# Performance work log

Hardware: AMD Instinct MI355X
Metric: run time of the kernel (lower is better)

## Reference

```python
import jax, jax.numpy as jnp
import numpy as np

N_NODES = 50000
N_EDGES = 800000
IN_CH = 256
HID = 64
OUT_CH = 64
N_LAYERS = 3
ALPHA = 0.1


def _gpr_temp():
    t = ALPHA * (1.0 - ALPHA) ** np.arange(N_LAYERS + 1)
    t[-1] = (1.0 - ALPHA) ** N_LAYERS
    return jnp.asarray(t, dtype=jnp.float32)


def setup_inputs() -> dict:
    key = jax.random.key(0)
    ks = jax.random.split(key, 8)
    x = jax.random.normal(ks[0], (N_NODES, IN_CH), dtype=jnp.float32)
    edge_index = jax.random.randint(ks[1], (2, N_EDGES), 0, N_NODES, dtype=jnp.int64 if jax.config.jax_enable_x64 else jnp.int32).astype(jnp.int32)
    edge_w = jax.random.uniform(ks[2], (N_EDGES,), dtype=jnp.float32)
    # xavier-uniform-ish scales
    W_in = jax.random.normal(ks[3], (IN_CH, HID), dtype=jnp.float32) * (1.0 / np.sqrt(IN_CH))
    b_in = jnp.zeros((HID,), dtype=jnp.float32)
    layer_W = jax.random.normal(ks[4], (N_LAYERS, HID, HID), dtype=jnp.float32) * (1.0 / np.sqrt(HID))
    layer_b = jnp.zeros((N_LAYERS, HID), dtype=jnp.float32)
    W_out = jax.random.normal(ks[5], (HID, OUT_CH), dtype=jnp.float32) * (1.0 / np.sqrt(HID))
    b_out = jnp.zeros((OUT_CH,), dtype=jnp.float32)
    temp = _gpr_temp()
    return {"x": x, "edge_index": edge_index, "edge_w": edge_w, "W_in": W_in,
            "b_in": b_in, "layer_W": layer_W, "layer_b": layer_b,
            "W_out": W_out, "b_out": b_out, "temp": temp}


def reference(x, edge_index, edge_w, W_in, b_in, layer_W, layer_b, W_out, b_out, temp):
    src, dst = edge_index[0], edge_index[1]
    # inlinear
    h = x @ W_in + b_in                      # [N, HID]
    # GPR combination: hidden = sum_k temp[k] * relu(SpMM(linear(h_k)))
    hidden = h * temp[0]
    cur = h
    for i in range(layer_W.shape[0]):
        z = cur @ layer_W[i] + layer_b[i]    # [N, HID]
        m = z[src] * edge_w[:, None]         # gather + edge weight, [E, HID]
        agg = jax.ops.segment_sum(m, dst, num_segments=x.shape[0])  # scatter-sum
        cur = jax.nn.relu(agg)               # dropout is identity in eval mode
        hidden = hidden + cur * temp[i + 1]
    return hidden @ W_out + b_out            # [N, OUT_CH]
```

## Files before the change

kernel.cpp:

```cpp
#include <hip/hip_runtime.h>
#include <hip/hip_bf16.h>

#define NN 50000
#define NE 800000
#define CIN 256
#define HH 64
#define NBINS 196
#define B1 256
#define EPB 3125
#define NGB 782
#define NLB 3125

typedef unsigned long long u64;
typedef __attribute__((ext_vector_type(8))) short short8;
typedef __attribute__((ext_vector_type(4))) float f32x4;

__device__ __forceinline__ float bf2f(ushort u) {
    union { unsigned int i; float f; } v; v.i = ((unsigned int)u) << 16; return v.f;
}
__device__ __forceinline__ ushort f2bf(float f) {
    __hip_bfloat16 b = __float2bfloat16(f);
    return *reinterpret_cast<ushort*>(&b);
}

__global__ __launch_bounds__(256) void k_prep(
    const float* __restrict__ W_in, const float* __restrict__ LW,
    const float* __restrict__ W_out, ushort* __restrict__ Wp)
{
    const int tid = blockIdx.x * 256 + threadIdx.x;
    if (tid < 16384) {
        const int i = tid & 7;
        const int l = (tid >> 3) & 63;
        const int s = (tid >> 9) & 7;
        const int t = tid >> 12;
        const int k = s * 32 + (l >> 4) * 8 + i;
        const int c = t * 16 + (l & 15);
        Wp[tid] = f2bf(W_in[k * HH + c]);
    } else {
        const int q = (tid - 16384) & 4095;
        const int m = (tid - 16384) >> 12;
        const int i = q & 7;
        const int l = (q >> 3) & 63;
        const int s = (q >> 9) & 1;
        const int t = q >> 10;
        const int k = s * 32 + (l >> 4) * 8 + i;
        const int c = t * 16 + (l & 15);
        const float* Wm = (m < 3) ? (LW + m * HH * HH) : W_out;
        Wp[tid] = f2bf(Wm[k * HH + c]);
    }
}

__global__ __launch_bounds__(256) void k_fused(
    const float* __restrict__ x, const ushort* __restrict__ Wp,
    const float* __restrict__ b, const int* __restrict__ dst,
    int* __restrict__ H, ushort* __restrict__ h_bf)
{
    __shared__ int hist[NBINS];
    if (blockIdx.x < B1) {
        for (int t = threadIdx.x; t < NBINS; t += 256) hist[t] = 0;
        __syncthreads();
        const int e0 = blockIdx.x * EPB;
        for (int i = threadIdx.x; i < EPB; i += 256)
            atomicAdd(&hist[dst[e0 + i] >> 8], 1);
        __syncthreads();
        for (int t = threadIdx.x; t < NBINS; t += 256)
            H[t * B1 + blockIdx.x] = hist[t];
        return;
    }
    const int w = threadIdx.x >> 6;
    const int l = threadIdx.x & 63;
    const int R0 = (blockIdx.x - B1) * 64 + w * 16;
    const int arow = R0 + (l & 15);
    const int xrow = (arow < NN) ? arow : (NN - 1);
    const float* xr = x + (size_t)xrow * CIN + (l >> 4) * 8;
    const short8* WpV = (const short8*)Wp;

    f32x4 acc0 = {0,0,0,0}, acc1 = {0,0,0,0}, acc2 = {0,0,0,0}, acc3 = {0,0,0,0};
    #pragma unroll
    for (int s = 0; s < 8; ++s) {
        const float4 xa = *(const float4*)(xr + s * 32);
        const float4 xb = *(const float4*)(xr + s * 32 + 4);
        short8 af;
        af[0] = (short)f2bf(xa.x); af[1] = (short)f2bf(xa.y);
        af[2] = (short)f2bf(xa.z); af[3] = (short)f2bf(xa.w);
        af[4] = (short)f2bf(xb.x); af[5] = (short)f2bf(xb.y);
        af[6] = (short)f2bf(xb.z); af[7] = (short)f2bf(xb.w);
        acc0 = __builtin_amdgcn_mfma_f32_16x16x32_bf16(af, WpV[(0*8+s)*64 + l], acc0, 0, 0, 0);
        acc1 = __builtin_amdgcn_mfma_f32_16x16x32_bf16(af, WpV[(1*8+s)*64 + l], acc1, 0, 0, 0);
        acc2 = __builtin_amdgcn_mfma_f32_16x16x32_bf16(af, WpV[(2*8+s)*64 + l], acc2, 0, 0, 0);
        acc3 = __builtin_amdgcn_mfma_f32_16x16x32_bf16(af, WpV[(3*8+s)*64 + l], acc3, 0, 0, 0);
    }
    const int colb = l & 15;
    const int rbase = R0 + (l >> 4) * 4;
    #pragma unroll
    for (int t = 0; t < 4; ++t) {
        const f32x4 a = (t == 0) ? acc0 : (t == 1) ? acc1 : (t == 2) ? acc2 : acc3;
        const float bb = b[t * 16 + colb];
        #pragma unroll
        for (int r = 0; r < 4; ++r) {
            const int row = rbase + r;
            if (row < NN)
                h_bf[(size_t)row * HH + t * 16 + colb] = f2bf(a[r] + bb);
        }
    }
}

__global__ __launch_bounds__(256) void k_scanH(
    int* __restrict__ H, int* __restrict__ Sx, int* __restrict__ bcnt)
{
    __shared__ int s[256];
    const int t = threadIdx.x;
    int rowsum = 0;
    if (t < NBINS) {
        const int4* row = (const int4*)(H + t * B1);
        #pragma unroll 8
        for (int c = 0; c < B1 / 4; ++c) {
            const int4 v = row[c];
            rowsum += v.x + v.y + v.z + v.w;
        }
    }
    s[t] = (t < NBINS) ? rowsum : 0;
    __syncthreads();
    #pragma unroll
    for (int off = 1; off < 256; off <<= 1) {
        const int add = (t >= off) ? s[t - off] : 0;
        __syncthreads();
        s[t] += add;
        __syncthreads();
    }
    if (t < NBINS) {
        const int rowstart = s[t] - rowsum;
        Sx[t] = rowstart;
        bcnt[t] = rowsum;
        int run = rowstart;
        int4* row = (int4*)(H + t * B1);
        for (int c = 0; c < B1 / 4; ++c) {
            int4 v = row[c];
            int4 o;
            o.x = run; run += v.x;
            o.y = run; run += v.y;
            o.z = run; run += v.z;
            o.w = run; run += v.w;
            row[c] = o;
        }
    }
}

__global__ __launch_bounds__(256) void k_scatterA(
    const int* __restrict__ src, const int* __restrict__ dst,
    const float* __restrict__ ew, const int* __restrict__ H,
    int2* __restrict__ tmp_e, ushort* __restrict__ tmp_low)
{
    __shared__ int cur[NBINS];
    for (int t = threadIdx.x; t < NBINS; t += 256)
        cur[t] = H[t * B1 + blockIdx.x];
    __syncthreads();
    const int e0 = blockIdx.x * EPB;
    for (int i = threadIdx.x; i < EPB; i += 256) {
        const int e = e0 + i;
        const int d = dst[e];
        const int pos = atomicAdd(&cur[d >> 8], 1);
        tmp_e[pos] = make_int2(src[e], __float_as_int(ew[e]));
        tmp_low[pos] = (ushort)(d & 255);
    }
}

__global__ __launch_bounds__(512) void k_sortB(
    const int2* __restrict__ tmp_e, const ushort* __restrict__ tmp_low,
    const int* __restrict__ Sx, const int* __restrict__ bcnt,
    int2* __restrict__ epack, int* __restrict__ rowptr, int* __restrict__ cnt)
{
    __shared__ int hist[256], s[256], curs[256];
    const int b = blockIdx.x;
    const int base = Sx[b];
    const int cntE = bcnt[b];
    const int t = threadIdx.x;
    if (t < 256) hist[t] = 0;
    __syncthreads();
    for (int i = t; i < cntE; i += 512)
        atomicAdd(&hist[tmp_low[base + i]], 1);
    __syncthreads();
    if (t < 256) s[t] = hist[t];
    __syncthreads();
    #pragma unroll
    for (int off = 1; off < 256; off <<= 1) {
        const int add = (t < 256 && t >= off) ? s[t - off] : 0;
        __syncthreads();
        if (t < 256) s[t] += add;
        __syncthreads();
    }
    if (t < 256) {
        const int excl = s[t] - hist[t];
        curs[t] = excl;
        const int d = b * 256 + t;
        if (d < NN) { rowptr[d] = base + excl; cnt[d] = hist[t]; }
    }
    __syncthreads();
    for (int i = t; i < cntE; i += 512) {
        const int2 e = tmp_e[base + i];
        const int low = (int)tmp_low[base + i];
        const int pos = base + atomicAdd(&curs[low], 1);
        epack[pos] = e;
    }
}

template<bool FINAL>
__global__ __launch_bounds__(256) void k_layer(
    const ushort* __restrict__ cur_in, ushort* __restrict__ cur_out,
    const int2* __restrict__ epack, const int* __restrict__ rowptr,
    const int* __restrict__ cnt,
    const ushort* __restrict__ WpL, const float* __restrict__ bvec,
    const float* __restrict__ temp,
    const ushort* __restrict__ hbf, const ushort* __restrict__ c1,
    const ushort* __restrict__ WpO, const float* __restrict__ bout,
    float* __restrict__ outp)
{
    __shared__ int2  es[4][64];
    __shared__ ushort ts[16][72];
    __shared__ float swv[16];
    const int w = threadIdx.x >> 6;
    const int j = threadIdx.x & 63;
    const int nb = blockIdx.x * 16;

    #pragma unroll
    for (int q = 0; q < 4; ++q) {
        const int n  = nb + w * 4 + q;
        const int rs = rowptr[n];
        const int rc = cnt[n];
        float acc = 0.0f;
        float sw  = 0.0f;
        for (int base = 0; base < rc; base += 64) {
            const int m = min(rc - base, 64);
            if (j < m) es[w][j] = epack[rs + base + j];
            for (int g = 0; g < m; g += 8) {
                float vv[8], ww[8];
                #pragma unroll
                for (int u = 0; u < 8; ++u) {
                    const int idx = g + u;
                    const int sel = (idx < m) ? idx : 0;
                    const int2 p = es[w][sel];
                    ww[u] = (idx < m) ? __int_as_float(p.y) : 0.0f;
                    vv[u] = bf2f(cur_in[(size_t)p.x * HH + j]);
                }
                #pragma unroll
                for (int u = 0; u < 8; ++u) { acc = fmaf(ww[u], vv[u], acc); sw += ww[u]; }
            }
        }
        ts[w * 4 + q][j] = f2bf(acc);
        if (j == 0) swv[w * 4 + q] = sw;
    }
    __syncthreads();

    const int lr = j & 15;
    const int lg = j >> 4;
    const short8 a0 = *(const short8*)&ts[lr][lg * 8];
    const short8 a1 = *(const short8*)&ts[lr][32 + lg * 8];
    if (FINAL) __syncthreads();

    const short8* WpV = (const short8*)WpL;
    f32x4 zac = {0,0,0,0};
    zac = __builtin_amdgcn_mfma_f32_16x16x32_bf16(a0, WpV[(w*2+0)*64 + j], zac, 0, 0, 0);
    zac = __builtin_amdgcn_mfma_f32_16x16x32_bf16(a1, WpV[(w*2+1)*64 + j], zac, 0, 0, 0);

    const float bb = bvec[w * 16 + lr];
    float t0v = 0, t1v = 0, t2v = 0, t3v = 0;
    if (FINAL) { t0v = temp[0]; t1v = temp[1]; t2v = temp[2]; t3v = temp[3]; }
    #pragma unroll
    for (int r = 0; r < 4; ++r) {
        const int row = lg * 4 + r;
        const int n   = nb + row;
        const float z = zac[r] + swv[row] * bb;
        const float rv = fmaxf(z, 0.0f);
        const size_t o = (size_t)n * HH + w * 16 + lr;
        if (!FINAL) {
            cur_out[o] = f2bf(rv);
        } else {
            const float hid = t0v * bf2f(hbf[o]) + t1v * bf2f(c1[o])
                            + t2v * bf2f(cur_in[o]) + t3v * rv;
            ts[row][w * 16 + lr] = f2bf(hid);
        }
    }
    if (FINAL) {
        __syncthreads();
        const short8 b0 = *(const short8*)&ts[lr][lg * 8];
        const short8 b1 = *(const short8*)&ts[lr][32 + lg * 8];
        const short8* WoV = (const short8*)WpO;
        f32x4 oz = {0,0,0,0};
        oz = __builtin_amdgcn_mfma_f32_16x16x32_bf16(b0, WoV[(w*2+0)*64 + j], oz, 0, 0, 0);
        oz = __builtin_amdgcn_mfma_f32_16x16x32_bf16(b1, WoV[(w*2+1)*64 + j], oz, 0, 0, 0);
        const float bo = bout[w * 16 + lr];
        #pragma unroll
        for (int r = 0; r < 4; ++r) {
            const int row = lg * 4 + r;
            outp[(size_t)(nb + row) * HH + w * 16 + lr] = oz[r] + bo;
        }
    }
}

extern "C" void kernel_launch(void* const* d_in, const int* in_sizes, int n_in,
                              void* d_out, int out_size, void* d_ws, size_t ws_size,
                              hipStream_t stream)
{
    const float* x     = (const float*)d_in[0];
    const int*   ei    = (const int*)d_in[1];
    const float* ew    = (const float*)d_in[2];
    const float* W_in  = (const float*)d_in[3];
    const float* b_in  = (const float*)d_in[4];
    const float* LW    = (const float*)d_in[5];
    const float* Lb    = (const float*)d_in[6];
    const float* W_out = (const float*)d_in[7];
    const float* b_out = (const float*)d_in[8];
    const float* temp  = (const float*)d_in[9];
    const int* src = ei;
    const int* dst = ei + NE;

    char* p = (char*)d_ws;
    ushort* h_bf    = (ushort*)p;  p += (size_t)NN * HH * 2;
    ushort* curA    = (ushort*)p;  p += (size_t)NN * HH * 2;
    ushort* curB    = (ushort*)p;  p += (size_t)NN * HH * 2;
    int2*   epack   = (int2*)p;    p += (size_t)NE * 8;
    int2*   tmp_e   = (int2*)p;    p += (size_t)NE * 8;
    ushort* tmp_low = (ushort*)p;  p += (size_t)NE * 2;
    int*    H       = (int*)p;     p += (size_t)NBINS * B1 * 4;
    int*    Sx      = (int*)p;     p += (NBINS + 1) * 4;
    int*    bcnt    = (int*)p;     p += NBINS * 4;
    int*    rowptr  = (int*)p;     p += (size_t)NN * 4;
    int*    cnt     = (int*)p;     p += (size_t)NN * 4;
    ushort* Wp      = (ushort*)p;  p += 32768 * 2;
    float*  out     = (float*)d_out;

    const ushort* WpIn  = Wp;
    const ushort* WpL0  = Wp + 16384;
    const ushort* WpL1  = Wp + 16384 + 4096;
    const ushort* WpL2  = Wp + 16384 + 2 * 4096;
    const ushort* WpOut = Wp + 16384 + 3 * 4096;

    k_prep<<<128, 256, 0, stream>>>(W_in, LW, W_out, Wp);
    k_fused<<<B1 + NGB, 256, 0, stream>>>(x, WpIn, b_in, dst, H, h_bf);
    k_scanH<<<1, 256, 0, stream>>>(H, Sx, bcnt);
    k_scatterA<<<B1, 256, 0, stream>>>(src, dst, ew, H, tmp_e, tmp_low);
    k_sortB<<<NBINS, 512, 0, stream>>>(tmp_e, tmp_low, Sx, bcnt, epack, rowptr, cnt);

    k_layer<false><<<NLB, 256, 0, stream>>>(h_bf, curA, epack, rowptr, cnt,
                                            WpL0, Lb + 0 * HH, temp,
                                            nullptr, nullptr, nullptr, nullptr, nullptr);
    k_layer<false><<<NLB, 256, 0, stream>>>(curA, curB, epack, rowptr, cnt,
                                            WpL1, Lb + 1 * HH, temp,
                                            nullptr, nullptr, nullptr, nullptr, nullptr);
    k_layer<true><<<NLB, 256, 0, stream>>>(curB, nullptr, epack, rowptr, cnt,
                                           WpL2, Lb + 2 * HH, temp,
                                           h_bf, curA, WpOut, b_out, out);
}
```

Before: 159.0 us.

## Parallelize histogram row scan across blocks and prefetch edge packs in layer kernel

The single-block scan that serially wrote per-bin offsets over 256 entries per thread is split in two. A one-block pass now computes only bin totals and starts, and a second 196-block pass does a parallel block-wide prefix scan of each histogram row. In the layer kernel, row pointers and counts for all four nodes are loaded up front, and each node's first 64 edge records are prefetched into a register while the previous node is aggregated, hiding epack load latency. The cost is an extra kernel launch, extra registers, and a clamped speculative load.

```diff
diff --git a/kernel.cpp b/kernel.cpp
--- a/kernel.cpp
+++ b/kernel.cpp
@@ -105,8 +105,8 @@
     }
 }
 
-__global__ __launch_bounds__(256) void k_scanH(
-    int* __restrict__ H, int* __restrict__ Sx, int* __restrict__ bcnt)
+__global__ __launch_bounds__(256) void k_scanS(
+    const int* __restrict__ H, int* __restrict__ Sx, int* __restrict__ bcnt)
 {
     __shared__ int s[256];
     const int t = threadIdx.x;
@@ -129,21 +129,28 @@
         __syncthreads();
     }
     if (t < NBINS) {
-        const int rowstart = s[t] - rowsum;
-        Sx[t] = rowstart;
+        Sx[t] = s[t] - rowsum;
         bcnt[t] = rowsum;
-        int run = rowstart;
-        int4* row = (int4*)(H + t * B1);
-        for (int c = 0; c < B1 / 4; ++c) {
-            int4 v = row[c];
-            int4 o;
-            o.x = run; run += v.x;
-            o.y = run; run += v.y;
-            o.z = run; run += v.z;
-            o.w = run; run += v.w;
-            row[c] = o;
-        }
-    }
+    }
+}
+
+__global__ __launch_bounds__(256) void k_scanW(
+    int* __restrict__ H, const int* __restrict__ Sx)
+{
+    __shared__ int s[256];
+    const int b = blockIdx.x;
+    const int t = threadIdx.x;
+    const int v = H[b * B1 + t];
+    s[t] = v;
+    __syncthreads();
+    #pragma unroll
+    for (int off = 1; off < 256; off <<= 1) {
+        const int add = (t >= off) ? s[t - off] : 0;
+        __syncthreads();
+        s[t] += add;
+        __syncthreads();
+    }
+    H[b * B1 + t] = s[t] - v + Sx[b];
 }
 
 __global__ __launch_bounds__(256) void k_scatterA(
@@ -222,14 +229,39 @@
     const int j = threadIdx.x & 63;
     const int nb = blockIdx.x * 16;
 
+    int rsA[4], rcA[4];
     #pragma unroll
     for (int q = 0; q < 4; ++q) {
-        const int n  = nb + w * 4 + q;
-        const int rs = rowptr[n];
-        const int rc = cnt[n];
+        rsA[q] = rowptr[nb + w * 4 + q];
+        rcA[q] = cnt[nb + w * 4 + q];
+    }
+    int2 pf = epack[min(rsA[0] + ((j < rcA[0]) ? j : 0), NE - 1)];
+
+    #pragma unroll
+    for (int q = 0; q < 4; ++q) {
+        const int rs = rsA[q];
+        const int rc = rcA[q];
+        es[w][j] = pf;
+        if (q < 3)
+            pf = epack[min(rsA[q+1] + ((j < rcA[q+1]) ? j : 0), NE - 1)];
+
         float acc = 0.0f;
         float sw  = 0.0f;
-        for (int base = 0; base < rc; base += 64) {
+        const int m0 = min(rc, 64);
+        for (int g = 0; g < m0; g += 8) {
+            float vv[8], ww[8];
+            #pragma unroll
+            for (int u = 0; u < 8; ++u) {
+                const int idx = g + u;
+                const int sel = (idx < m0) ? idx : 0;
+                const int2 p = es[w][sel];
+                ww[u] = (idx < m0) ? __int_as_float(p.y) : 0.0f;
+                vv[u] = bf2f(cur_in[(size_t)p.x * HH + j]);
+            }
+            #pragma unroll
+            for (int u = 0; u < 8; ++u) { acc = fmaf(ww[u], vv[u], acc); sw += ww[u]; }
+        }
+        for (int base = 64; base < rc; base += 64) {
             const int m = min(rc - base, 64);
             if (j < m) es[w][j] = epack[rs + base + j];
             for (int g = 0; g < m; g += 8) {
@@ -337,7 +369,8 @@
 
     k_prep<<<128, 256, 0, stream>>>(W_in, LW, W_out, Wp);
     k_fused<<<B1 + NGB, 256, 0, stream>>>(x, WpIn, b_in, dst, H, h_bf);
-    k_scanH<<<1, 256, 0, stream>>>(H, Sx, bcnt);
+    k_scanS<<<1, 256, 0, stream>>>(H, Sx, bcnt);
+    k_scanW<<<NBINS, 256, 0, stream>>>(H, Sx);
     k_scatterA<<<B1, 256, 0, stream>>>(src, dst, ew, H, tmp_e, tmp_low);
     k_sortB<<<NBINS, 512, 0, stream>>>(tmp_e, tmp_low, Sx, bcnt, epack, rowptr, cnt);
 
```

After: 135.2 us. -15.0%, faster.
